# Kernel tuning notes

Measured on AMD Instinct MI355X. Metric: run time of the kernel, lower is better.

## Reference

```python
import jax, jax.numpy as jnp
import numpy as np
from jax import lax

C, H, W = 256, 56, 56
KP, STRIDE = 9, 2
M_CH, D, T = 64, 128, 16
TOPK = 32
SIGMA, ALPHA, TAU, EPS = 3.0, 10.0, 10.0, 1e-6
B = 4
N = H * W
PAD = KP // 2


def _build_M_P(h, w, s):
    ys = np.arange(0, h, s)
    xs = np.arange(0, w, s)
    ny, nx = len(ys), len(xs)
    N_, K_ = h * w, ny * nx
    by, bx = np.meshgrid(np.arange(h, dtype=np.float32), np.arange(w, dtype=np.float32), indexing='ij')
    bx = bx.reshape(-1)
    by = by.reshape(-1)
    fx, fy = bx / float(s), by / float(s)
    x0 = np.floor(fx).astype(np.int64)
    y0 = np.floor(fy).astype(np.int64)
    x0c = np.clip(x0, 0, nx - 1)
    x1c = np.clip(x0 + 1, 0, nx - 1)
    y0c = np.clip(y0, 0, ny - 1)
    y1c = np.clip(y0 + 1, 0, ny - 1)
    wx = fx - x0
    wy = fy - y0
    Mm = np.zeros((N_, K_), dtype=np.float32)
    rows = np.arange(N_)
    Mm[rows, y0c * nx + x0c] += (1 - wx) * (1 - wy)
    Mm[rows, y0c * nx + x1c] += wx * (1 - wy)
    Mm[rows, y1c * nx + x0c] += (1 - wx) * wy
    Mm[rows, y1c * nx + x1c] += wx * wy
    rs = Mm.sum(1, keepdims=True)
    rs[rs == 0] = 1.0
    Mm = Mm / rs
    P = np.stack([bx, by], axis=-1).astype(np.float32)  # (N,2) (x,y)
    return Mm, P


def _forward(feature_map, A_bank, pw_w, pw_b, proj_w, proj_b, r, M, P):
    def make_grid(A):  # affine_grid, align_corners=False
        xs = (2.0 * jnp.arange(W, dtype=jnp.float32) + 1.0) / W - 1.0
        ys = (2.0 * jnp.arange(H, dtype=jnp.float32) + 1.0) / H - 1.0
        gy, gx = jnp.meshgrid(ys, xs, indexing='ij')
        base = jnp.stack([gx, gy, jnp.ones_like(gx)], axis=-1)  # (H,W,3)
        return base @ A.T  # (H,W,2) normalized (x,y)

    def grid_sample(grid):  # bilinear, border padding, align_corners=False
        ix = ((grid[..., 0] + 1.0) * W - 1.0) / 2.0
        iy = ((grid[..., 1] + 1.0) * H - 1.0) / 2.0
        x0 = jnp.floor(ix)
        y0 = jnp.floor(iy)
        wx = ix - x0
        wy = iy - y0
        x0c = jnp.clip(x0, 0, W - 1).astype(jnp.int32)
        x1c = jnp.clip(x0 + 1, 0, W - 1).astype(jnp.int32)
        y0c = jnp.clip(y0, 0, H - 1).astype(jnp.int32)
        y1c = jnp.clip(y0 + 1, 0, H - 1).astype(jnp.int32)
        fm = feature_map.reshape(B, C, H * W)
        def g(yc, xc):
            return fm[:, :, (yc * W + xc).reshape(-1)].reshape(B, C, H, W)
        return (g(y0c, x0c) * (1 - wx) * (1 - wy) + g(y0c, x1c) * wx * (1 - wy)
                + g(y1c, x0c) * (1 - wx) * wy + g(y1c, x1c) * wx * wy)

    grids = jax.vmap(make_grid)(A_bank)          # (T,H,W,2)
    warped = jax.vmap(grid_sample)(grids)        # (T,B,C,H,W)

    # unfold(k,pad,stride) -> 1x1 conv -> spatial mean  ==  zero-padded avg-pool then linear
    pm = lax.reduce_window(warped, 0.0, lax.add,
                           (1, 1, 1, KP, KP), (1, 1, 1, STRIDE, STRIDE),
                           [(0, 0), (0, 0), (0, 0), (PAD, PAD), (PAD, PAD)]) / (KP * KP)
    Tn, Bn, Cn, Kh, Kw = pm.shape
    K = Kh * Kw
    pm = pm.reshape(Tn, Bn, Cn, K).transpose(0, 1, 3, 2)  # (T,B,K,C)
    x = pm @ pw_w.T + pw_b                                 # (T,B,K,m)
    z = x @ proj_w.T + proj_b                              # (T,B,K,d)
    z = z / jnp.maximum(jnp.linalg.norm(z, axis=-1, keepdims=True), EPS)
    Z = z.transpose(1, 0, 2, 3)                            # (B,T,K,d)

    s = jnp.einsum('btkd,d->btk', Z, r)
    wgt = jax.nn.softmax(TAU * s, axis=1)[..., None]
    g_emb = jnp.sum(wgt * Z, axis=1)                       # (B,K,d)

    E = jnp.einsum('nk,bkd->bnd', M, g_emb)
    E = E / jnp.maximum(jnp.linalg.norm(E, axis=-1, keepdims=True), EPS)

    d2 = jnp.sum((P[:, None, :] - P[None, :, :]) ** 2, axis=-1)  # (N,N)
    G = 1.0 - jnp.exp(-d2 / (2.0 * SIGMA ** 2))
    Saff = jnp.einsum('bnd,bmd->bnm', E, E) * G

    vals, idx = lax.top_k(Saff, TOPK)
    bidx = jnp.arange(B)[:, None, None]
    nidx = jnp.arange(N)[None, :, None]
    S_sp = jnp.zeros_like(Saff).at[bidx, nidx, idx].set(vals)
    A0 = jax.nn.softmax(ALPHA * S_sp, axis=-1) * jax.nn.softmax(ALPHA * S_sp, axis=-2)
    return E, A0


def setup_inputs() -> dict:
    key = jax.random.key(0)
    ks = jax.random.split(key, 6)
    feature_map = jax.random.normal(ks[0], (B, C, H, W), jnp.float32)
    ident = jnp.broadcast_to(jnp.array([[1.0, 0.0, 0.0], [0.0, 1.0, 0.0]], jnp.float32), (T, 2, 3))
    A_bank = ident + 0.1 * jax.random.normal(ks[1], (T, 2, 3), jnp.float32)
    pw_w = jax.random.normal(ks[2], (M_CH, C), jnp.float32) / np.sqrt(C).astype(np.float32)
    pw_b = jnp.zeros((M_CH,), jnp.float32)
    proj_w = jax.random.normal(ks[3], (D, M_CH), jnp.float32) / np.sqrt(M_CH).astype(np.float32)
    proj_b = jnp.zeros((D,), jnp.float32)
    r = 0.01 * jax.random.normal(ks[4], (D,), jnp.float32)
    Mnp, Pnp = _build_M_P(H, W, STRIDE)
    return {'feature_map': feature_map, 'A_bank': A_bank, 'pw_w': pw_w, 'pw_b': pw_b,
            'proj_w': proj_w, 'proj_b': proj_b, 'r': r,
            'M': jnp.asarray(Mnp), 'P': jnp.asarray(Pnp)}


def reference(feature_map, A_bank, pw_w, pw_b, proj_w, proj_b, r, M, P):
    return _forward(feature_map, A_bank, pw_w, pw_b, proj_w, proj_b, r, M, P)
```

## Files before the change

kernel.cpp:

```cpp
#include <hip/hip_runtime.h>
#include <hip/hip_bf16.h>
#include <hip/hip_fp16.h>

#define Hh 56
#define Ww 56
#define Cc 256
#define Tt 16
#define Bb 4
#define Nn 3136
#define Kk 784
#define KX 28
#define Dd 128
#define Mc 64
#define NTOP 32

typedef __attribute__((ext_vector_type(8))) _Float16 f16x8;
typedef __attribute__((ext_vector_type(4))) float f32x4;

__global__ __launch_bounds__(256) void k_prep(
    const float* __restrict__ pw_w, const float* __restrict__ pw_b,
    const float* __restrict__ proj_w, const float* __restrict__ proj_b,
    const float* __restrict__ Abank,
    float* __restrict__ wct, float* __restrict__ bc,
    unsigned* __restrict__ offo, float2* __restrict__ wo,
    float* __restrict__ dc) {
  int blk = blockIdx.x;
  if (blk < 256) {
    int c = blk;
    int d = threadIdx.x;
    if (d < 128) {
      float acc = 0.f;
      for (int m = 0; m < Mc; ++m) acc += proj_w[d * Mc + m] * pw_w[m * Cc + c];
      wct[c * Dd + d] = acc;
      if (c == 0) {
        float bb = proj_b[d];
        for (int m = 0; m < Mc; ++m) bb += proj_w[d * Mc + m] * pw_b[m];
        bc[d] = bb;
      }
    }
  } else if (blk < 272) {
    int t = blk - 256;
    const float* A = Abank + t * 6;
    float a00 = A[0], a01 = A[1], a02 = A[2], a10 = A[3], a11 = A[4], a12 = A[5];
    for (int e = threadIdx.x; e < Nn; e += 256) {
      int h = e / 56, w = e - h * 56;
      float gx = (2.0f * w + 1.0f) / 56.0f - 1.0f;
      float gy = (2.0f * h + 1.0f) / 56.0f - 1.0f;
      float u = a00 * gx + a01 * gy + a02;
      float v = a10 * gx + a11 * gy + a12;
      float ix = ((u + 1.0f) * 56.0f - 1.0f) * 0.5f;
      float iy = ((v + 1.0f) * 56.0f - 1.0f) * 0.5f;
      float x0f = floorf(ix), y0f = floorf(iy);
      int x0 = (int)x0f, y0 = (int)y0f;
      int x0c = min(max(x0, 0), 55), x1c = min(max(x0 + 1, 0), 55);
      int y0c = min(max(y0, 0), 55), y1c = min(max(y0 + 1, 0), 55);
      offo[t * Nn + e] = (y0c * 56 + x0c) | ((x1c - x0c) << 12) | ((y1c - y0c) << 13);
      float2 wv2;
      wv2.x = ix - x0f;
      wv2.y = iy - y0f;
      wo[t * Nn + e] = wv2;
    }
  } else {
    int i = (blk - 272) * 256 + threadIdx.x;
    if (i < Bb * Nn) dc[i] = (float)Nn;
  }
}

__global__ __launch_bounds__(256) void k_mix(
    const float* __restrict__ fm, const float* __restrict__ wct, float* __restrict__ y) {
  int blk = blockIdx.x;
  int b = blk / 98;
  int n0 = (blk % 98) * 32;
  int tid = threadIdx.x;
  int d = tid & 127;
  int ng = tid >> 7;
  __shared__ __align__(16) float fm_s[64][32];
  __shared__ float wc_s[64 * Dd];
  float acc[16];
#pragma unroll
  for (int j = 0; j < 16; ++j) acc[j] = 0.f;
  const float* fb = fm + (size_t)b * Cc * Nn;
  for (int c0 = 0; c0 < Cc; c0 += 64) {
    for (int i = tid; i < 64 * 32; i += 256) {
      int c = i >> 5, kx = i & 31;
      fm_s[c][kx] = fb[(size_t)(c0 + c) * Nn + n0 + kx];
    }
    for (int i = tid; i < 64 * Dd; i += 256) wc_s[i] = wct[c0 * Dd + i];
    __syncthreads();
    for (int c = 0; c < 64; ++c) {
      float w = wc_s[c * Dd + d];
      const float4* fr = reinterpret_cast<const float4*>(&fm_s[c][ng * 16]);
      float4 f0 = fr[0], f1 = fr[1], f2 = fr[2], f3 = fr[3];
      acc[0]  += f0.x * w; acc[1]  += f0.y * w; acc[2]  += f0.z * w; acc[3]  += f0.w * w;
      acc[4]  += f1.x * w; acc[5]  += f1.y * w; acc[6]  += f1.z * w; acc[7]  += f1.w * w;
      acc[8]  += f2.x * w; acc[9]  += f2.y * w; acc[10] += f2.z * w; acc[11] += f2.w * w;
      acc[12] += f3.x * w; acc[13] += f3.y * w; acc[14] += f3.z * w; acc[15] += f3.w * w;
    }
    __syncthreads();
  }
  size_t base = (((size_t)b * 64 + (d >> 1)) * Nn + n0 + ng * 16) * 2 + (d & 1);
#pragma unroll
  for (int j = 0; j < 16; ++j) y[base + 2 * j] = acc[j];
}

__global__ __launch_bounds__(256) void k_fused_pool(
    const float* __restrict__ yraw, const unsigned* __restrict__ offo,
    const float2* __restrict__ wo, const float* __restrict__ bc,
    float* __restrict__ zt) {
  const float2* y2 = reinterpret_cast<const float2*>(yraw);
  int idx = blockIdx.x;
  int b = idx & 3;
  int pg = (idx >> 2) & 15;
  int t = idx >> 6;
  __shared__ float2 wsm[3136];
  __shared__ float2 rowp[1568];
  int tid = threadIdx.x;
  const unsigned* offp = offo + t * Nn;
  const float2* wp = wo + t * Nn;
  unsigned off[13];
  float2 wv[13];
#pragma unroll
  for (int j = 0; j < 13; ++j) {
    int e = tid + 256 * j;
    if (e < 3136) {
      off[j] = offp[e];
      wv[j] = wp[e];
    }
  }
  for (int pp = 0; pp < 4; ++pp) {
    int dp = pg * 4 + pp;
    const float2* fc = y2 + ((size_t)b * 64 + dp) * Nn;
    float b0 = bc[dp * 2], b1 = bc[dp * 2 + 1];
#pragma unroll
    for (int j = 0; j < 13; ++j) {
      int e = tid + 256 * j;
      if (e < 3136) {
        unsigned pk = off[j];
        int base = pk & 4095;
        int dx = (pk >> 12) & 1;
        int dyy = (pk & (1u << 13)) ? 56 : 0;
        float2 v00 = fc[base], v01 = fc[base + dx];
        float2 v10 = fc[base + dyy], v11 = fc[base + dyy + dx];
        float wx = wv[j].x, wy = wv[j].y;
        float tx = v00.x + wx * (v01.x - v00.x);
        float bx = v10.x + wx * (v11.x - v10.x);
        float ty = v00.y + wx * (v01.y - v00.y);
        float by = v10.y + wx * (v11.y - v10.y);
        float2 o;
        o.x = tx + wy * (bx - tx);
        o.y = ty + wy * (by - ty);
        wsm[e] = o;
      }
    }
    __syncthreads();
    for (int e = tid; e < 1568; e += 256) {
      int h = e / 28, kx = e - h * 28;
      int xs = 2 * kx - 4;
      int lo = max(xs, 0), hi = min(xs + 8, 55);
      float sx = 0.f, sy = 0.f;
      const float2* wr = wsm + h * 56;
      for (int x = lo; x <= hi; ++x) { float2 v = wr[x]; sx += v.x; sy += v.y; }
      float2 o; o.x = sx; o.y = sy;
      rowp[e] = o;
    }
    __syncthreads();
    float* zo0 = zt + ((size_t)(t * Bb + b) * Dd + dp * 2) * Kk;
    float* zo1 = zo0 + Kk;
    for (int e = tid; e < 784; e += 256) {
      int ky = e / 28, kx = e - ky * 28;
      int ys = 2 * ky - 4;
      int lo = max(ys, 0), hi = min(ys + 8, 55);
      float sx = 0.f, sy = 0.f;
      for (int h = lo; h <= hi; ++h) { float2 rv = rowp[h * 28 + kx]; sx += rv.x; sy += rv.y; }
      zo0[e] = sx * (1.0f / 81.0f) + b0;
      zo1[e] = sy * (1.0f / 81.0f) + b1;
    }
    __syncthreads();
  }
}

__global__ __launch_bounds__(256) void k_znorm(
    const float* __restrict__ zt, const float* __restrict__ r,
    float* __restrict__ z, float* __restrict__ s_arr) {
  int tb = blockIdx.x / 14;
  int k0 = (blockIdx.x % 14) * 56;
  int tid = threadIdx.x;
  __shared__ float ls[56 * 129];
  const float* zb = zt + (size_t)tb * Dd * Kk + k0;
  for (int i = tid; i < Dd * 56; i += 256) {
    int d = i / 56, kk = i - d * 56;
    ls[kk * 129 + d] = zb[(size_t)d * Kk + kk];
  }
  int lane = tid & 63;
  int wvv = tid >> 6;
  float r0 = r[lane], r1 = r[lane + 64];
  __syncthreads();
  for (int p = 0; p < 14; ++p) {
    int k = p * 4 + wvv;
    float z0 = ls[k * 129 + lane];
    float z1 = ls[k * 129 + 64 + lane];
    float ss = z0 * z0 + z1 * z1;
    for (int off = 32; off; off >>= 1) ss += __shfl_xor(ss, off);
    float inv = 1.0f / fmaxf(sqrtf(ss), 1e-6f);
    z0 *= inv; z1 *= inv;
    float* zr = z + ((size_t)tb * Kk + k0 + k) * Dd;
    zr[lane] = z0;
    zr[lane + 64] = z1;
    float sd = z0 * r0 + z1 * r1;
    for (int off = 32; off; off >>= 1) sd += __shfl_xor(sd, off);
    if (lane == 0) s_arr[(size_t)tb * Kk + k0 + k] = sd;
  }
}

__global__ __launch_bounds__(128) void k_gemb(
    const float* __restrict__ z, const float* __restrict__ s_arr, float* __restrict__ g) {
  int blk = blockIdx.x;
  int b = blk / Kk, k = blk % Kk;
  int d = threadIdx.x;
  float sv[Tt];
  float mx = -3.4e38f;
#pragma unroll
  for (int t = 0; t < Tt; ++t) {
    sv[t] = s_arr[(t * Bb + b) * Kk + k];
    mx = fmaxf(mx, sv[t]);
  }
  float sum = 0.f;
#pragma unroll
  for (int t = 0; t < Tt; ++t) {
    sv[t] = expf(10.0f * (sv[t] - mx));
    sum += sv[t];
  }
  float isum = 1.0f / sum;
  float acc = 0.f;
#pragma unroll
  for (int t = 0; t < Tt; ++t)
    acc += sv[t] * isum * z[((size_t)(t * Bb + b) * Kk + k) * Dd + d];
  g[((size_t)b * Kk + k) * Dd + d] = acc;
}

__global__ __launch_bounds__(128) void k_E(
    const float* __restrict__ Mmat, const float* __restrict__ g,
    float* __restrict__ E, _Float16* __restrict__ E16) {
  int row = blockIdx.x * 2 + (threadIdx.x >> 6);
  int b = row / Nn, n = row % Nn;
  int y = n / Ww, x = n % Ww;
  int x0 = x >> 1, y0 = y >> 1;
  int x1 = min(x0 + 1, 27), y1 = min(y0 + 1, 27);
  bool hx = (x1 != x0), hy = (y1 != y0);
  int k00 = y0 * 28 + x0, k01 = y0 * 28 + x1, k10 = y1 * 28 + x0, k11 = y1 * 28 + x1;
  const float* Mr = Mmat + (size_t)n * Kk;
  float m00 = Mr[k00];
  float m01 = hx ? Mr[k01] : 0.f;
  float m10 = hy ? Mr[k10] : 0.f;
  float m11 = (hx && hy) ? Mr[k11] : 0.f;
  const float* gb = g + (size_t)b * Kk * Dd;
  int lane = threadIdx.x & 63;
  int l2 = lane + 64;
  float a0 = m00 * gb[k00 * Dd + lane] + m01 * gb[k01 * Dd + lane] +
             m10 * gb[k10 * Dd + lane] + m11 * gb[k11 * Dd + lane];
  float a1 = m00 * gb[k00 * Dd + l2] + m01 * gb[k01 * Dd + l2] +
             m10 * gb[k10 * Dd + l2] + m11 * gb[k11 * Dd + l2];
  float ss = a0 * a0 + a1 * a1;
  for (int off = 32; off; off >>= 1) ss += __shfl_xor(ss, off);
  float inv = 1.0f / fmaxf(sqrtf(ss), 1e-6f);
  float e0 = a0 * inv, e1 = a1 * inv;
  E[(size_t)row * Dd + lane] = e0;
  E[(size_t)row * Dd + l2] = e1;
  E16[(size_t)row * Dd + lane] = (_Float16)e0;
  E16[(size_t)row * Dd + l2] = (_Float16)e1;
}

__global__ __launch_bounds__(256) void k_saff(
    const _Float16* __restrict__ E16, __half* __restrict__ S) {
  int blk = blockIdx.x;
  int b = blk / 1225;
  int rem = blk % 1225;
  int ti0 = (int)((sqrtf(8.f * rem + 1.f) - 1.f) * 0.5f);
  while ((ti0 + 1) * (ti0 + 2) / 2 <= rem) ++ti0;
  while (ti0 * (ti0 + 1) / 2 > rem) --ti0;
  int tj0 = rem - ti0 * (ti0 + 1) / 2;
  int i0 = ti0 * 64, j0 = tj0 * 64;
  int wave = threadIdx.x >> 6, lane = threadIdx.x & 63;
  int wr = wave >> 1, wc = wave & 1;
  int lr = lane & 15, lk = lane >> 4;
  int ibase = i0 + wr * 32;
  int jbase = j0 + wc * 32;
  const _Float16* Eb = E16 + (size_t)b * Nn * Dd;
  __shared__ __half tileT[64][66];
  __shared__ __half tileR[64][66];
  f32x4 acc00 = {0.f, 0.f, 0.f, 0.f};
  f32x4 acc01 = acc00, acc10 = acc00, acc11 = acc00;
#pragma unroll
  for (int ks = 0; ks < 4; ++ks) {
    int ko = ks * 32 + lk * 8;
    f16x8 a0 = *reinterpret_cast<const f16x8*>(Eb + (size_t)(ibase + lr) * Dd + ko);
    f16x8 a1 = *reinterpret_cast<const f16x8*>(Eb + (size_t)(ibase + 16 + lr) * Dd + ko);
    f16x8 b0 = *reinterpret_cast<const f16x8*>(Eb + (size_t)(jbase + lr) * Dd + ko);
    f16x8 b1 = *reinterpret_cast<const f16x8*>(Eb + (size_t)(jbase + 16 + lr) * Dd + ko);
    acc00 = __builtin_amdgcn_mfma_f32_16x16x32_f16(a0, b0, acc00, 0, 0, 0);
    acc01 = __builtin_amdgcn_mfma_f32_16x16x32_f16(a0, b1, acc01, 0, 0, 0);
    acc10 = __builtin_amdgcn_mfma_f32_16x16x32_f16(a1, b0, acc10, 0, 0, 0);
    acc11 = __builtin_amdgcn_mfma_f32_16x16x32_f16(a1, b1, acc11, 0, 0, 0);
  }
  size_t ob = (size_t)b * Nn * Nn;
  int gj[2];
  float xj[2], yj[2];
#pragma unroll
  for (int tj = 0; tj < 2; ++tj) {
    gj[tj] = jbase + tj * 16 + lr;
    int yv = gj[tj] / 56;
    yj[tj] = (float)yv;
    xj[tj] = (float)(gj[tj] - yv * 56);
  }
  bool mirror = (i0 != j0);
#pragma unroll
  for (int ti = 0; ti < 2; ++ti) {
#pragma unroll
    for (int q = 0; q < 4; ++q) {
      int iloc = wr * 32 + ti * 16 + lk * 4 + q;
      int gi = i0 + iloc;
      int yiv = gi / 56;
      float yi = (float)yiv;
      float xi = (float)(gi - yiv * 56);
#pragma unroll
      for (int tj = 0; tj < 2; ++tj) {
        float a;
        if (ti == 0 && tj == 0) a = acc00[q];
        else if (ti == 0 && tj == 1) a = acc01[q];
        else if (ti == 1 && tj == 0) a = acc10[q];
        else a = acc11[q];
        float dx = xi - xj[tj];
        float dy = yi - yj[tj];
        float gg = 1.0f - __expf(-(dx * dx + dy * dy) * (1.0f / 18.0f));
        __half hv = __float2half(a * gg);
        int jloc = wc * 32 + tj * 16 + lr;
        tileR[iloc][jloc] = hv;
        tileT[jloc][iloc] = hv;
      }
    }
  }
  __syncthreads();
  for (int e = threadIdx.x; e < 64 * 32; e += 256) {
    int row = e >> 5, c2 = e & 31;
    unsigned v = *reinterpret_cast<const unsigned*>(&tileR[row][c2 * 2]);
    *reinterpret_cast<unsigned*>(&S[ob + (size_t)(i0 + row) * Nn + j0 + c2 * 2]) = v;
  }
  if (mirror) {
    for (int e = threadIdx.x; e < 64 * 32; e += 256) {
      int row = e >> 5, c2 = e & 31;
      unsigned v = *reinterpret_cast<const unsigned*>(&tileT[row][c2 * 2]);
      *reinterpret_cast<unsigned*>(&S[ob + (size_t)(j0 + row) * Nn + i0 + c2 * 2]) = v;
    }
  }
}

__global__ __launch_bounds__(256) void k_topk(
    const __half* __restrict__ S16, const float* __restrict__ E,
    const float* __restrict__ P, float* __restrict__ topv, int* __restrict__ topi,
    float* __restrict__ dr, float* __restrict__ dc) {
  int row = blockIdx.x;
  int b = row / Nn, irow = row % Nn;
  int tid = threadIdx.x;
  const unsigned* Sr = reinterpret_cast<const unsigned*>(S16 + (size_t)row * Nn);
  __shared__ unsigned hist[256 * 8];
  __shared__ unsigned wtot[4];
  __shared__ unsigned bcast[2];
  __shared__ unsigned sel_eq, sel_slot;
  __shared__ int sel_idx[NTOP];
  __shared__ float drow_s;
  unsigned pk[7];
#pragma unroll
  for (int j = 0; j < 7; ++j) {
    int c2 = tid + 256 * j;
    unsigned u = (c2 < Nn / 2) ? Sr[c2] : 0u;
    unsigned h0 = u & 0xFFFFu, h1 = u >> 16;
    unsigned k0 = h0 ^ ((h0 & 0x8000u) ? 0xFFFFu : 0x8000u);
    unsigned k1 = h1 ^ ((h1 & 0x8000u) ? 0xFFFFu : 0x8000u);
    if (c2 >= Nn / 2) { k0 = 0u; k1 = 0u; }
    pk[j] = k0 | (k1 << 16);
  }
  if (tid == 0) { sel_eq = 0; sel_slot = 0; drow_s = 0.f; }
  int lane = tid & 63, wvq = tid >> 6;
  unsigned prefix = 0;
  unsigned k = NTOP;
  for (int pass = 0; pass < 2; ++pass) {
    int shift = 8 - 8 * pass;
    unsigned pmask = pass ? 0xFF00u : 0u;
#pragma unroll
    for (int i = 0; i < 8; ++i) hist[tid * 8 + i] = 0;
    __syncthreads();
#pragma unroll
    for (int j = 0; j < 7; ++j) {
      unsigned k0 = pk[j] & 0xFFFFu, k1 = pk[j] >> 16;
      if ((k0 & pmask) == (prefix & pmask))
        atomicAdd(&hist[((k0 >> shift) & 255u) * 8 + (tid & 7)], 1u);
      if ((k1 & pmask) == (prefix & pmask))
        atomicAdd(&hist[((k1 >> shift) & 255u) * 8 + (tid & 7)], 1u);
    }
    __syncthreads();
    unsigned cnt = 0;
#pragma unroll
    for (int i = 0; i < 8; ++i) cnt += hist[tid * 8 + i];
    unsigned run = cnt;
#pragma unroll
    for (int off2 = 1; off2 < 64; off2 <<= 1) {
      unsigned v = __shfl_down(run, off2);
      if (lane + off2 < 64) run += v;
    }
    if (lane == 0) wtot[wvq] = run;
    __syncthreads();
    unsigned hi = 0;
    for (int w2 = wvq + 1; w2 < 4; ++w2) hi += wtot[w2];
    unsigned incl = run + hi;
    unsigned excl = incl - cnt;
    if (excl < k && k <= incl) {
      bcast[0] = prefix | ((unsigned)tid << shift);
      bcast[1] = k - excl;
    }
    __syncthreads();
    prefix = bcast[0];
    k = bcast[1];
    __syncthreads();
  }
  unsigned T = prefix;
#pragma unroll
  for (int j = 0; j < 7; ++j) {
    int c2 = tid + 256 * j;
    if (c2 < Nn / 2) {
      unsigned k0 = pk[j] & 0xFFFFu, k1 = pk[j] >> 16;
      bool take0 = (k0 > T) || (k0 == T && atomicAdd(&sel_eq, 1u) < k);
      if (take0) { unsigned slot = atomicAdd(&sel_slot, 1u); sel_idx[slot] = 2 * c2; }
      bool take1 = (k1 > T) || (k1 == T && atomicAdd(&sel_eq, 1u) < k);
      if (take1) { unsigned slot = atomicAdd(&sel_slot, 1u); sel_idx[slot] = 2 * c2 + 1; }
    }
  }
  __syncthreads();
  int sel = tid >> 3, part = tid & 7;
  int col = sel_idx[sel];
  const float* Ei = E + ((size_t)b * Nn + irow) * Dd;
  const float* Ej = E + ((size_t)b * Nn + col) * Dd;
  float v = 0.f;
#pragma unroll
  for (int d0 = 0; d0 < 16; ++d0) {
    int d = part * 16 + d0;
    v += Ei[d] * Ej[d];
  }
  v += __shfl_xor(v, 1);
  v += __shfl_xor(v, 2);
  v += __shfl_xor(v, 4);
  if (part == 0) {
    float dx = P[irow * 2] - P[col * 2];
    float dy = P[irow * 2 + 1] - P[col * 2 + 1];
    float gg = 1.0f - __expf(-(dx * dx + dy * dy) * (1.0f / 18.0f));
    v *= gg;
    topv[(size_t)row * NTOP + sel] = v;
    topi[(size_t)row * NTOP + sel] = col;
    float e = __expf(10.f * v);
    atomicAdd(&dc[b * Nn + col], e - 1.f);
    atomicAdd(&drow_s, e);
  }
  __syncthreads();
  if (tid == 0) dr[row] = (float)(Nn - NTOP) + drow_s;
}

__global__ void k_inv(float* __restrict__ dr, float* __restrict__ dc) {
  int i = blockIdx.x * 256 + threadIdx.x;
  if (i < Bb * Nn) {
    dr[i] = 1.0f / dr[i];
    dc[i] = 1.0f / dc[i];
  }
}

__global__ __launch_bounds__(256) void k_basefix(
    const float* __restrict__ invdr, const float* __restrict__ invdc,
    const float* __restrict__ topv, const int* __restrict__ topi,
    float* __restrict__ A0) {
  int row = blockIdx.x;
  int b = row / Nn;
  float idr = invdr[row];
  const float4* dc4 = reinterpret_cast<const float4*>(invdc + b * Nn);
  float4* out4 = reinterpret_cast<float4*>(A0 + (size_t)row * Nn);
  for (int j = threadIdx.x; j < Nn / 4; j += 256) {
    float4 c = dc4[j];
    float4 o = {idr * c.x, idr * c.y, idr * c.z, idr * c.w};
    out4[j] = o;
  }
  __syncthreads();
  if (threadIdx.x < NTOP) {
    int gidx = row * NTOP + threadIdx.x;
    int col = topi[gidx];
    float e = __expf(10.f * topv[gidx]);
    A0[(size_t)row * Nn + col] = e * e * idr * invdc[b * Nn + col];
  }
}

extern "C" void kernel_launch(void* const* d_in, const int* in_sizes, int n_in,
                              void* d_out, int out_size, void* d_ws, size_t ws_size,
                              hipStream_t stream) {
  const float* fm     = (const float*)d_in[0];
  const float* Abank  = (const float*)d_in[1];
  const float* pw_w   = (const float*)d_in[2];
  const float* pw_b   = (const float*)d_in[3];
  const float* proj_w = (const float*)d_in[4];
  const float* proj_b = (const float*)d_in[5];
  const float* r      = (const float*)d_in[6];
  const float* Mmat   = (const float*)d_in[7];
  const float* P      = (const float*)d_in[8];
  float* out = (float*)d_out;
  float* E  = out;
  float* A0 = out + (size_t)Bb * Nn * Dd;
  __half* S16 = (__half*)A0;

  float* ws = (float*)d_ws;
  float* y     = ws;
  float* zt    = ws + 1605632;
  float* z     = ws + 8028160;
  float* wct   = ws + 14450688;
  float* bcv   = ws + 14483456;
  float* s_arr = ws + 14483584;
  float* g     = ws + 14533760;
  float* topv  = ws + 14935168;
  int*   topi  = (int*)(ws + 15336576);
  float* dr    = ws + 15737984;
  float* dc    = ws + 15750528;
  _Float16* E16 = (_Float16*)(ws + 15763072);
  unsigned* offo = (unsigned*)(ws + 16565888);
  float2*   wo   = (float2*)(ws + 16616064);

  hipLaunchKernelGGL(k_prep, dim3(321), dim3(256), 0, stream,
                     pw_w, pw_b, proj_w, proj_b, Abank, wct, bcv, offo, wo, dc);
  hipLaunchKernelGGL(k_mix, dim3(392), dim3(256), 0, stream, fm, wct, y);
  hipLaunchKernelGGL(k_fused_pool, dim3(1024), dim3(256), 0, stream, y, offo, wo, bcv, zt);
  hipLaunchKernelGGL(k_znorm, dim3(64 * 14), dim3(256), 0, stream, zt, r, z, s_arr);
  hipLaunchKernelGGL(k_gemb, dim3(Bb * Kk), dim3(128), 0, stream, z, s_arr, g);
  hipLaunchKernelGGL(k_E, dim3(Bb * Nn / 2), dim3(128), 0, stream, Mmat, g, E, E16);
  hipLaunchKernelGGL(k_saff, dim3(Bb * 1225), dim3(256), 0, stream, E16, S16);
  hipLaunchKernelGGL(k_topk, dim3(Bb * Nn), dim3(256), 0, stream, S16, E, P, topv, topi, dr, dc);
  hipLaunchKernelGGL(k_inv, dim3(49), dim3(256), 0, stream, dr, dc);
  hipLaunchKernelGGL(k_basefix, dim3(Bb * Nn), dim3(256), 0, stream, dr, dc, topv, topi, A0);
}
```

Before: 434.0 us.

## Split pooling over output row bands, write S directly, fold reciprocal into basefix

The fused pool kernel now splits each (t,b) map into four bands of seven output rows plus halo, with two channel pairs per block instead of four. This raises the grid from 1024 to 8192 blocks and shrinks shared memory, at the cost of recomputing halo rows. The affinity kernel writes the non-mirrored S tile straight from registers with scalar half stores and keeps only the transposed tile in LDS. The separate reciprocal kernel is removed and its divisions are done inside basefix, trading one launch for per-element divides.

```diff
diff --git a/kernel.cpp b/kernel.cpp
--- a/kernel.cpp
+++ b/kernel.cpp
@@ -103,75 +103,73 @@
   for (int j = 0; j < 16; ++j) y[base + 2 * j] = acc[j];
 }
 
-__global__ __launch_bounds__(256) void k_fused_pool(
+__global__ __launch_bounds__(256, 8) void k_fused_pool(
     const float* __restrict__ yraw, const unsigned* __restrict__ offo,
     const float2* __restrict__ wo, const float* __restrict__ bc,
     float* __restrict__ zt) {
   const float2* y2 = reinterpret_cast<const float2*>(yraw);
   int idx = blockIdx.x;
   int b = idx & 3;
-  int pg = (idx >> 2) & 15;
-  int t = idx >> 6;
-  __shared__ float2 wsm[3136];
-  __shared__ float2 rowp[1568];
+  int pg = (idx >> 2) & 31;
+  int t = (idx >> 7) & 15;
+  int kq = idx >> 11;
+  int ky0 = kq * 7;
+  int hlo = max(0, 2 * ky0 - 4);
+  int hhi = min(55, 2 * ky0 + 16);
+  int nh = hhi - hlo + 1;
+  __shared__ float2 wsm[21 * 56];
+  __shared__ float2 rowp[21 * 28];
   int tid = threadIdx.x;
-  const unsigned* offp = offo + t * Nn;
-  const float2* wp = wo + t * Nn;
-  unsigned off[13];
-  float2 wv[13];
-#pragma unroll
-  for (int j = 0; j < 13; ++j) {
-    int e = tid + 256 * j;
-    if (e < 3136) {
-      off[j] = offp[e];
-      wv[j] = wp[e];
-    }
-  }
-  for (int pp = 0; pp < 4; ++pp) {
-    int dp = pg * 4 + pp;
+  const unsigned* offp = offo + t * Nn + hlo * 56;
+  const float2* wp = wo + t * Nn + hlo * 56;
+  int npix = nh * 56;
+  int nrp = nh * 28;
+  for (int pp = 0; pp < 2; ++pp) {
+    int dp = pg * 2 + pp;
     const float2* fc = y2 + ((size_t)b * 64 + dp) * Nn;
     float b0 = bc[dp * 2], b1 = bc[dp * 2 + 1];
-#pragma unroll
-    for (int j = 0; j < 13; ++j) {
-      int e = tid + 256 * j;
-      if (e < 3136) {
-        unsigned pk = off[j];
-        int base = pk & 4095;
-        int dx = (pk >> 12) & 1;
-        int dyy = (pk & (1u << 13)) ? 56 : 0;
-        float2 v00 = fc[base], v01 = fc[base + dx];
-        float2 v10 = fc[base + dyy], v11 = fc[base + dyy + dx];
-        float wx = wv[j].x, wy = wv[j].y;
-        float tx = v00.x + wx * (v01.x - v00.x);
-        float bx = v10.x + wx * (v11.x - v10.x);
-        float ty = v00.y + wx * (v01.y - v00.y);
-        float by = v10.y + wx * (v11.y - v10.y);
-        float2 o;
-        o.x = tx + wy * (bx - tx);
-        o.y = ty + wy * (by - ty);
-        wsm[e] = o;
-      }
-    }
-    __syncthreads();
-    for (int e = tid; e < 1568; e += 256) {
-      int h = e / 28, kx = e - h * 28;
+    for (int e = tid; e < npix; e += 256) {
+      unsigned pk = offp[e];
+      int base = pk & 4095;
+      int dx = (pk >> 12) & 1;
+      int dyy = (pk & (1u << 13)) ? 56 : 0;
+      float2 v00 = fc[base], v01 = fc[base + dx];
+      float2 v10 = fc[base + dyy], v11 = fc[base + dyy + dx];
+      float2 wv = wp[e];
+      float wx = wv.x, wy = wv.y;
+      float tx = v00.x + wx * (v01.x - v00.x);
+      float bx = v10.x + wx * (v11.x - v10.x);
+      float ty = v00.y + wx * (v01.y - v00.y);
+      float by = v10.y + wx * (v11.y - v10.y);
+      float2 o;
+      o.x = tx + wy * (bx - tx);
+      o.y = ty + wy * (by - ty);
+      wsm[e] = o;
+    }
+    __syncthreads();
+    for (int e = tid; e < nrp; e += 256) {
+      int lh = e / 28, kx = e - lh * 28;
       int xs = 2 * kx - 4;
       int lo = max(xs, 0), hi = min(xs + 8, 55);
       float sx = 0.f, sy = 0.f;
-      const float2* wr = wsm + h * 56;
+      const float2* wr = wsm + lh * 56;
       for (int x = lo; x <= hi; ++x) { float2 v = wr[x]; sx += v.x; sy += v.y; }
       float2 o; o.x = sx; o.y = sy;
       rowp[e] = o;
     }
     __syncthreads();
-    float* zo0 = zt + ((size_t)(t * Bb + b) * Dd + dp * 2) * Kk;
+    float* zo0 = zt + ((size_t)(t * Bb + b) * Dd + dp * 2) * Kk + ky0 * 28;
     float* zo1 = zo0 + Kk;
-    for (int e = tid; e < 784; e += 256) {
-      int ky = e / 28, kx = e - ky * 28;
+    for (int e = tid; e < 7 * 28; e += 256) {
+      int kyl = e / 28, kx = e - kyl * 28;
+      int ky = ky0 + kyl;
       int ys = 2 * ky - 4;
       int lo = max(ys, 0), hi = min(ys + 8, 55);
       float sx = 0.f, sy = 0.f;
-      for (int h = lo; h <= hi; ++h) { float2 rv = rowp[h * 28 + kx]; sx += rv.x; sy += rv.y; }
+      for (int h = lo; h <= hi; ++h) {
+        float2 rv = rowp[(h - hlo) * 28 + kx];
+        sx += rv.x; sy += rv.y;
+      }
       zo0[e] = sx * (1.0f / 81.0f) + b0;
       zo1[e] = sy * (1.0f / 81.0f) + b1;
     }
@@ -286,8 +284,7 @@
   int ibase = i0 + wr * 32;
   int jbase = j0 + wc * 32;
   const _Float16* Eb = E16 + (size_t)b * Nn * Dd;
-  __shared__ __half tileT[64][66];
-  __shared__ __half tileR[64][66];
+  __shared__ __half tile[64][66];
   f32x4 acc00 = {0.f, 0.f, 0.f, 0.f};
   f32x4 acc01 = acc00, acc10 = acc00, acc11 = acc00;
 #pragma unroll
@@ -333,22 +330,17 @@
         float dy = yi - yj[tj];
         float gg = 1.0f - __expf(-(dx * dx + dy * dy) * (1.0f / 18.0f));
         __half hv = __float2half(a * gg);
+        S[ob + (size_t)gi * Nn + gj[tj]] = hv;
         int jloc = wc * 32 + tj * 16 + lr;
-        tileR[iloc][jloc] = hv;
-        tileT[jloc][iloc] = hv;
+        tile[jloc][iloc] = hv;
       }
     }
   }
-  __syncthreads();
-  for (int e = threadIdx.x; e < 64 * 32; e += 256) {
-    int row = e >> 5, c2 = e & 31;
-    unsigned v = *reinterpret_cast<const unsigned*>(&tileR[row][c2 * 2]);
-    *reinterpret_cast<unsigned*>(&S[ob + (size_t)(i0 + row) * Nn + j0 + c2 * 2]) = v;
-  }
   if (mirror) {
+    __syncthreads();
     for (int e = threadIdx.x; e < 64 * 32; e += 256) {
       int row = e >> 5, c2 = e & 31;
-      unsigned v = *reinterpret_cast<const unsigned*>(&tileT[row][c2 * 2]);
+      unsigned v = *reinterpret_cast<const unsigned*>(&tile[row][c2 * 2]);
       *reinterpret_cast<unsigned*>(&S[ob + (size_t)(j0 + row) * Nn + i0 + c2 * 2]) = v;
     }
   }
@@ -463,26 +455,18 @@
   if (tid == 0) dr[row] = (float)(Nn - NTOP) + drow_s;
 }
 
-__global__ void k_inv(float* __restrict__ dr, float* __restrict__ dc) {
-  int i = blockIdx.x * 256 + threadIdx.x;
-  if (i < Bb * Nn) {
-    dr[i] = 1.0f / dr[i];
-    dc[i] = 1.0f / dc[i];
-  }
-}
-
 __global__ __launch_bounds__(256) void k_basefix(
-    const float* __restrict__ invdr, const float* __restrict__ invdc,
+    const float* __restrict__ dr, const float* __restrict__ dc,
     const float* __restrict__ topv, const int* __restrict__ topi,
     float* __restrict__ A0) {
   int row = blockIdx.x;
   int b = row / Nn;
-  float idr = invdr[row];
-  const float4* dc4 = reinterpret_cast<const float4*>(invdc + b * Nn);
+  float idr = 1.0f / dr[row];
+  const float4* dc4 = reinterpret_cast<const float4*>(dc + b * Nn);
   float4* out4 = reinterpret_cast<float4*>(A0 + (size_t)row * Nn);
   for (int j = threadIdx.x; j < Nn / 4; j += 256) {
     float4 c = dc4[j];
-    float4 o = {idr * c.x, idr * c.y, idr * c.z, idr * c.w};
+    float4 o = {idr / c.x, idr / c.y, idr / c.z, idr / c.w};
     out4[j] = o;
   }
   __syncthreads();
@@ -490,7 +474,7 @@
     int gidx = row * NTOP + threadIdx.x;
     int col = topi[gidx];
     float e = __expf(10.f * topv[gidx]);
-    A0[(size_t)row * Nn + col] = e * e * idr * invdc[b * Nn + col];
+    A0[(size_t)row * Nn + col] = e * e * idr / dc[b * Nn + col];
   }
 }
 
@@ -530,12 +514,11 @@
   hipLaunchKernelGGL(k_prep, dim3(321), dim3(256), 0, stream,
                      pw_w, pw_b, proj_w, proj_b, Abank, wct, bcv, offo, wo, dc);
   hipLaunchKernelGGL(k_mix, dim3(392), dim3(256), 0, stream, fm, wct, y);
-  hipLaunchKernelGGL(k_fused_pool, dim3(1024), dim3(256), 0, stream, y, offo, wo, bcv, zt);
+  hipLaunchKernelGGL(k_fused_pool, dim3(8192), dim3(256), 0, stream, y, offo, wo, bcv, zt);
   hipLaunchKernelGGL(k_znorm, dim3(64 * 14), dim3(256), 0, stream, zt, r, z, s_arr);
   hipLaunchKernelGGL(k_gemb, dim3(Bb * Kk), dim3(128), 0, stream, z, s_arr, g);
   hipLaunchKernelGGL(k_E, dim3(Bb * Nn / 2), dim3(128), 0, stream, Mmat, g, E, E16);
   hipLaunchKernelGGL(k_saff, dim3(Bb * 1225), dim3(256), 0, stream, E16, S16);
   hipLaunchKernelGGL(k_topk, dim3(Bb * Nn), dim3(256), 0, stream, S16, E, P, topv, topi, dr, dc);
-  hipLaunchKernelGGL(k_inv, dim3(49), dim3(256), 0, stream, dr, dc);
   hipLaunchKernelGGL(k_basefix, dim3(Bb * Nn), dim3(256), 0, stream, dr, dc, topv, topi, A0);
 }
```

Measured after the change: 415.7 us. 4.2% less time.
